# Optimization experiments

Hardware: AMD Instinct MI355X
Metric: run time of the kernel (lower is better)

Reference implementation:

```python
import jax, jax.numpy as jnp
import numpy as np

N_NODES = 50000
N_EDGES = 1600000
D = 64


def setup_inputs() -> dict:
    key = jax.random.key(0)
    ks = jax.random.split(key, 7)
    scale = 1.0 / np.sqrt(2 * D)  # keep activations sane through relu stack
    x = jax.random.normal(ks[0], (N_NODES, D), dtype=jnp.float32)
    edge_index = jax.random.randint(ks[1], (2, N_EDGES), 0, N_NODES, dtype=jnp.int32)
    edge_weight = jax.random.uniform(ks[2], (N_EDGES,), dtype=jnp.float32)
    W1 = jax.random.normal(ks[3], (D, 2 * D), dtype=jnp.float32) * scale
    b1 = jax.random.normal(ks[4], (D,), dtype=jnp.float32) * 0.01
    W2 = jax.random.normal(ks[5], (D, 2 * D), dtype=jnp.float32) * scale
    b2 = jax.random.normal(ks[6], (D,), dtype=jnp.float32) * 0.01
    return {"x": x, "edge_index": edge_index, "edge_weight": edge_weight,
            "W1": W1, "b1": b1, "W2": W2, "b2": b2}


def _sage_conv(x, src, dst, edge_weight, W, b):
    # gather neighbor features, weight, scatter-mean onto src nodes
    m = x[dst] * edge_weight[:, None]                      # [E, d]
    agg_sum = jax.ops.segment_sum(m, src, num_segments=x.shape[0])
    cnt = jax.ops.segment_sum(jnp.ones_like(edge_weight), src,
                              num_segments=x.shape[0])
    agg = agg_sum / jnp.maximum(cnt, 1.0)[:, None]          # scatter 'mean'
    h = jnp.concatenate([x, agg], axis=1)                   # [N, 2d]
    return h @ W.T + b


def reference(x, edge_index, edge_weight, W1, b1, W2, b2):
    src, dst = edge_index[0], edge_index[1]
    h = jax.nn.relu(_sage_conv(x, src, dst, edge_weight, W1, b1))
    h = jax.nn.relu(_sage_conv(h, src, dst, edge_weight, W2, b2))
    return h
```

## Files before the change

kernel.cpp:

```cpp
#include <hip/hip_runtime.h>

#define NN 50000
#define NE 1600000
#define DD 64
#define NPB 196
#define NBKT 256
#define CHUNK 2500
#define NBLK 640
#define SLOT 24
#define SSTR 25
#define S1CAP 1024
#define SPCAP 512
#define CSRCAP 8192

typedef __attribute__((ext_vector_type(8))) short bf16x8;
typedef __attribute__((ext_vector_type(4))) float f32x4;
typedef __attribute__((ext_vector_type(2))) float f32x2;

static __device__ __forceinline__ unsigned short f2bf(float f) {
    unsigned int u = __float_as_uint(f);
    unsigned int r = (u + 0x7FFFu + ((u >> 16) & 1u)) >> 16;
    return (unsigned short)r;
}
static __device__ __forceinline__ float bf2f(unsigned short h) {
    return __uint_as_float((unsigned int)h << 16);
}
static __device__ __forceinline__ unsigned int pk_fp8x4(float a, float b, float c, float d) {
    unsigned int p = __builtin_amdgcn_cvt_pk_fp8_f32(a, b, 0u, false);
    p = __builtin_amdgcn_cvt_pk_fp8_f32(c, d, p, true);
    return p;
}

__global__ __launch_bounds__(256) void prep(
    const float* __restrict__ x, ushort* __restrict__ xb,
    unsigned int* __restrict__ xf8,
    const float* __restrict__ W1, const float* __restrict__ W2,
    ushort* __restrict__ W1b, ushort* __restrict__ W2b,
    int* __restrict__ gcur)
{
    int b = blockIdx.x, tid = threadIdx.x;
    if (b < 3125) {
        int i = b * 256 + tid;
        float4 v = ((const float4*)x)[i];
        ushort4 o;
        o.x = f2bf(v.x); o.y = f2bf(v.y); o.z = f2bf(v.z); o.w = f2bf(v.w);
        ((ushort4*)xb)[i] = o;
        xf8[i] = pk_fp8x4(v.x, v.y, v.z, v.w);
    } else if (b < 3141) {
        int i = (b - 3125) * 256 + tid;
        const float* src = (i < 2048) ? W1 : W2;
        ushort* dst = (i < 2048) ? W1b : W2b;
        int j = i & 2047;
        float4 v = ((const float4*)src)[j];
        ushort4 o;
        o.x = f2bf(v.x); o.y = f2bf(v.y); o.z = f2bf(v.z); o.w = f2bf(v.w);
        ((ushort4*)dst)[j] = o;
    } else {
        for (int i = tid; i < 2304; i += 256) gcur[i] = 0;
    }
}

__global__ __launch_bounds__(256) void bin_lds(
    const int* __restrict__ ei, const float* __restrict__ ew,
    int* __restrict__ gcur, int* __restrict__ gspillc,
    int2* __restrict__ buf1, int2* __restrict__ spill)
{
    __shared__ int2 slot[NBKT * SSTR];
    __shared__ int  lcnt[NBKT];
    __shared__ int  lbase[NBKT];
    int tid = threadIdx.x;
    int shard = blockIdx.x & 7;

    for (int b = tid; b < NBKT; b += 256) lcnt[b] = 0;
    __syncthreads();

    int e0 = blockIdx.x * CHUNK;
    for (int i = tid; i < CHUNK; i += 256) {
        int e = e0 + i;
        int s = ei[e];
        int d = ei[NE + e];
        float w = ew[e];
        int bkt = s / NPB;
        int sloc = s - bkt * NPB;
        int2 rec = make_int2(d | ((int)f2bf(w) << 16), sloc);
        int pos = atomicAdd(&lcnt[bkt], 1);
        if (pos < SLOT) {
            slot[bkt * SSTR + pos] = rec;
        } else {
            int sp = atomicAdd(&gspillc[bkt], 1);
            if (sp < SPCAP) spill[bkt * SPCAP + sp] = rec;
        }
    }
    __syncthreads();

    {
        int b = tid;
        int n = lcnt[b]; if (n > SLOT) n = SLOT;
        lcnt[b] = n;
        lbase[b] = (n > 0) ? atomicAdd(&gcur[b * 8 + shard], n) : 0;
    }
    __syncthreads();

    int wave = tid >> 6, lane = tid & 63;
    int b0 = wave * 64;
    int vcnt = lcnt[b0 + lane];
    int vbase = lbase[b0 + lane];
#pragma unroll 8
    for (int j = 0; j < 64; ++j) {
        int n = __shfl(vcnt, j);
        int base = __shfl(vbase, j);
        int b = b0 + j;
        if (lane < n) {
            int2 rec = slot[b * SSTR + lane];
            int p = base + lane;
            if (p < S1CAP) {
                buf1[((size_t)b * 8 + shard) * S1CAP + p] = rec;
            } else {
                int sp = atomicAdd(&gspillc[b], 1);
                if (sp < SPCAP) spill[b * SPCAP + sp] = rec;
            }
        }
    }
}

__global__ __launch_bounds__(1024) void build_csr(
    const int* __restrict__ gcur, const int2* __restrict__ buf1,
    const int* __restrict__ gspillc, const int2* __restrict__ spill,
    unsigned int* __restrict__ csr, int2* __restrict__ rc)
{
    __shared__ int lcnt[NPB];
    __shared__ int lstart[NPB];
    __shared__ int sa[256], sb[256];
    int tid = threadIdx.x, bkt = blockIdx.x;

    if (tid < NPB) lcnt[tid] = 0;
    __syncthreads();

    for (int sh = 0; sh < 9; ++sh) {
        int n; const int2* rp;
        if (sh < 8) {
            n = gcur[bkt * 8 + sh]; if (n > S1CAP) n = S1CAP;
            rp = buf1 + ((size_t)bkt * 8 + sh) * S1CAP;
        } else {
            n = gspillc[bkt]; if (n > SPCAP) n = SPCAP;
            rp = spill + (size_t)bkt * SPCAP;
        }
        for (int i = tid; i < n; i += 1024)
            atomicAdd(&lcnt[rp[i].y], 1);
    }
    __syncthreads();

    if (tid < 256) sa[tid] = (tid < NPB) ? ((lcnt[tid] + 3) & ~3) : 0;
    __syncthreads();
    int* s = sa; int* d = sb;
    for (int off = 1; off < 256; off <<= 1) {
        if (tid < 256) d[tid] = s[tid] + (tid >= off ? s[tid - off] : 0);
        __syncthreads();
        int* t = s; s = d; d = t;
    }
    if (tid < NPB) {
        int ex = (tid == 0) ? 0 : s[tid - 1];
        lstart[tid] = ex;
        int node = bkt * NPB + tid;
        if (node < NN)
            rc[node] = make_int2(bkt * CSRCAP + ex, lcnt[tid]);
    }
    __syncthreads();
    if (tid < NPB) lcnt[tid] = 0;
    __syncthreads();

    for (int sh = 0; sh < 9; ++sh) {
        int n; const int2* rp;
        if (sh < 8) {
            n = gcur[bkt * 8 + sh]; if (n > S1CAP) n = S1CAP;
            rp = buf1 + ((size_t)bkt * 8 + sh) * S1CAP;
        } else {
            n = gspillc[bkt]; if (n > SPCAP) n = SPCAP;
            rp = spill + (size_t)bkt * SPCAP;
        }
        for (int i = tid; i < n; i += 1024) {
            int2 r = rp[i];
            int pos = atomicAdd(&lcnt[r.y], 1);
            csr[bkt * CSRCAP + lstart[r.y] + pos] = (unsigned int)r.x;
        }
    }
    __syncthreads();

    if (tid < NPB) {
        int c = lcnt[tid];
        int c4 = (c + 3) & ~3;
        for (int p = c; p < c4; ++p)
            csr[bkt * CSRCAP + lstart[tid] + p] = 0u;
    }
}

__global__ __launch_bounds__(256) void aggregate(
    const unsigned int* __restrict__ f8,
    const int2* __restrict__ rc, const unsigned int* __restrict__ csr,
    ushort* __restrict__ aggb)
{
    int node = (blockIdx.x * 256 + threadIdx.x) >> 6;
    int lane = threadIdx.x & 63;
    int g = lane >> 4, l16 = lane & 15;
    int2 rcv = rc[node];
    int n = rcv.y;
    int n4 = (n + 3) & ~3;
    const unsigned int* __restrict__ rp = csr + rcv.x;
    float a0 = 0.f, a1 = 0.f, a2 = 0.f, a3 = 0.f;

    int i = 0;
    for (; i + 16 <= n4; i += 16) {
        uint4 r = *(const uint4*)(rp + i + g * 4);
        unsigned int v0 = f8[(r.x & 0xFFFF) * 16 + l16];
        unsigned int v1 = f8[(r.y & 0xFFFF) * 16 + l16];
        unsigned int v2 = f8[(r.z & 0xFFFF) * 16 + l16];
        unsigned int v3 = f8[(r.w & 0xFFFF) * 16 + l16];
        float w0 = bf2f((unsigned short)(r.x >> 16));
        float w1 = bf2f((unsigned short)(r.y >> 16));
        float w2 = bf2f((unsigned short)(r.z >> 16));
        float w3 = bf2f((unsigned short)(r.w >> 16));
        f32x2 lo, hi;
        lo = __builtin_amdgcn_cvt_pk_f32_fp8(v0, false);
        hi = __builtin_amdgcn_cvt_pk_f32_fp8(v0, true);
        a0 += w0 * lo.x; a1 += w0 * lo.y; a2 += w0 * hi.x; a3 += w0 * hi.y;
        lo = __builtin_amdgcn_cvt_pk_f32_fp8(v1, false);
        hi = __builtin_amdgcn_cvt_pk_f32_fp8(v1, true);
        a0 += w1 * lo.x; a1 += w1 * lo.y; a2 += w1 * hi.x; a3 += w1 * hi.y;
        lo = __builtin_amdgcn_cvt_pk_f32_fp8(v2, false);
        hi = __builtin_amdgcn_cvt_pk_f32_fp8(v2, true);
        a0 += w2 * lo.x; a1 += w2 * lo.y; a2 += w2 * hi.x; a3 += w2 * hi.y;
        lo = __builtin_amdgcn_cvt_pk_f32_fp8(v3, false);
        hi = __builtin_amdgcn_cvt_pk_f32_fp8(v3, true);
        a0 += w3 * lo.x; a1 += w3 * lo.y; a2 += w3 * hi.x; a3 += w3 * hi.y;
    }
    for (; i < n4; i += 4) {
        uint4 r = *(const uint4*)(rp + i);
        unsigned int e = (g == 0) ? r.x : (g == 1) ? r.y : (g == 2) ? r.z : r.w;
        unsigned int v = f8[(e & 0xFFFF) * 16 + l16];
        float w = bf2f((unsigned short)(e >> 16));
        f32x2 lo = __builtin_amdgcn_cvt_pk_f32_fp8(v, false);
        f32x2 hi = __builtin_amdgcn_cvt_pk_f32_fp8(v, true);
        a0 += w * lo.x; a1 += w * lo.y; a2 += w * hi.x; a3 += w * hi.y;
    }

    a0 += __shfl_xor(a0, 16); a0 += __shfl_xor(a0, 32);
    a1 += __shfl_xor(a1, 16); a1 += __shfl_xor(a1, 32);
    a2 += __shfl_xor(a2, 16); a2 += __shfl_xor(a2, 32);
    a3 += __shfl_xor(a3, 16); a3 += __shfl_xor(a3, 32);

    if (lane < 16) {
        float dm = (float)(n > 1 ? n : 1);
        ushort4 o;
        o.x = f2bf(a0 / dm); o.y = f2bf(a1 / dm);
        o.z = f2bf(a2 / dm); o.w = f2bf(a3 / dm);
        *(ushort4*)&aggb[(size_t)node * DD + l16 * 4] = o;
    }
}

__global__ __launch_bounds__(256) void sage_gemm_mfma(
    const ushort* __restrict__ X, const ushort* __restrict__ A,
    const ushort* __restrict__ Wb, const float* __restrict__ bias,
    float* __restrict__ out, ushort* __restrict__ outb,
    unsigned char* __restrict__ outf8)
{
    int tid = threadIdx.x;
    int wave = tid >> 6, lane = tid & 63;
    int quad = lane >> 4, l16 = lane & 15;
    int m0 = blockIdx.x * 64 + wave * 16;

    int arow = m0 + l16; if (arow >= NN) arow = NN - 1;
    const ushort* __restrict__ ax = X + (size_t)arow * DD;
    const ushort* __restrict__ aa = A + (size_t)arow * DD;

    f32x4 acc[4];
#pragma unroll
    for (int t = 0; t < 4; ++t) acc[t] = (f32x4){0.f, 0.f, 0.f, 0.f};

#pragma unroll
    for (int ki = 0; ki < 4; ++ki) {
        const ushort* ap = (ki < 2) ? (ax + ki * 32 + quad * 8)
                                    : (aa + (ki - 2) * 32 + quad * 8);
        bf16x8 af = *(const bf16x8*)ap;
#pragma unroll
        for (int t = 0; t < 4; ++t) {
            const ushort* bp = Wb + (size_t)(t * 16 + l16) * 128 + ki * 32 + quad * 8;
            bf16x8 bfrag = *(const bf16x8*)bp;
            acc[t] = __builtin_amdgcn_mfma_f32_16x16x32_bf16(af, bfrag, acc[t], 0, 0, 0);
        }
    }

#pragma unroll
    for (int t = 0; t < 4; ++t) {
        int col = t * 16 + l16;
        float bv = bias[col];
#pragma unroll
        for (int r = 0; r < 4; ++r) {
            int grow = m0 + quad * 4 + r;
            if (grow < NN) {
                float v = fmaxf(acc[t][r] + bv, 0.f);
                if (out)  out[(size_t)grow * DD + col] = v;
                if (outb) outb[(size_t)grow * DD + col] = f2bf(v);
                if (outf8) {
                    unsigned int p = __builtin_amdgcn_cvt_pk_fp8_f32(v, v, 0u, false);
                    outf8[(size_t)grow * DD + col] = (unsigned char)(p & 0xFFu);
                }
            }
        }
    }
}

extern "C" void kernel_launch(void* const* d_in, const int* in_sizes, int n_in,
                              void* d_out, int out_size, void* d_ws, size_t ws_size,
                              hipStream_t stream)
{
    const float* x  = (const float*)d_in[0];
    const int*   ei = (const int*)d_in[1];
    const float* ew = (const float*)d_in[2];
    const float* W1 = (const float*)d_in[3];
    const float* b1 = (const float*)d_in[4];
    const float* W2 = (const float*)d_in[5];
    const float* b2 = (const float*)d_in[6];
    float* out = (float*)d_out;

    char* ws = (char*)d_ws;
    int*          gcur    = (int*)ws;
    int*          gspillc = (int*)(ws + 8192);
    int2*         buf1    = (int2*)(ws + 16384);
    int2*         spill   = (int2*)(ws + 16793600);
    unsigned int* csr     = (unsigned int*)(ws + 17842176);
    int2*         rc      = (int2*)(ws + 26230784);
    ushort*       xb      = (ushort*)(ws + 26632192);
    ushort*       aggb    = (ushort*)(ws + 33032192);
    ushort*       h1b     = (ushort*)(ws + 39432192);
    ushort*       W1b     = (ushort*)(ws + 45832192);
    ushort*       W2b     = (ushort*)(ws + 45848576);
    unsigned int* xf8     = (unsigned int*)(ws + 45864960);
    unsigned char* h1f8   = (unsigned char*)(ws + 49064960);

    prep<<<3142, 256, 0, stream>>>(x, xb, xf8, W1, W2, W1b, W2b, gcur);
    bin_lds<<<NBLK, 256, 0, stream>>>(ei, ew, gcur, gspillc, buf1, spill);
    build_csr<<<NBKT, 1024, 0, stream>>>(gcur, buf1, gspillc, spill, csr, rc);

    aggregate<<<(NN * 64) / 256, 256, 0, stream>>>(xf8, rc, csr, aggb);
    sage_gemm_mfma<<<(NN + 63) / 64, 256, 0, stream>>>(xb, aggb, W1b, b1, nullptr, h1b, h1f8);

    aggregate<<<(NN * 64) / 256, 256, 0, stream>>>((const unsigned int*)h1f8, rc, csr, aggb);
    sage_gemm_mfma<<<(NN + 63) / 64, 256, 0, stream>>>(h1b, aggb, W2b, b2, out, nullptr, nullptr);
}
```

Baseline: 202.2 us.

## Fuse neighbor aggregation with MFMA linear layer per 16-node block

Merges the aggregate and GEMM kernels into one 1024-thread kernel. Each of its 16 waves aggregates one node into LDS, then 4 waves run the 16x64 MFMA tile from LDS. This removes the aggb global round trip and two kernel launches per layer. In exchange, 12 of 16 waves sit idle during the GEMM phase, blocks sync on their slowest node's degree, and every block reloads the weight fragments.

After: 199.2 us. No clear change (-1.5%).

```diff
diff --git a/kernel.cpp b/kernel.cpp
--- a/kernel.cpp
+++ b/kernel.cpp
@@ -194,14 +194,26 @@
     }
 }
 
-__global__ __launch_bounds__(256) void aggregate(
+__global__ __launch_bounds__(1024) void fused_layer(
+    const ushort* __restrict__ Xb,
     const unsigned int* __restrict__ f8,
     const int2* __restrict__ rc, const unsigned int* __restrict__ csr,
-    ushort* __restrict__ aggb)
-{
-    int node = (blockIdx.x * 256 + threadIdx.x) >> 6;
-    int lane = threadIdx.x & 63;
+    const ushort* __restrict__ Wb, const float* __restrict__ bias,
+    float* __restrict__ out, ushort* __restrict__ outb,
+    unsigned char* __restrict__ outf8)
+{
+    __shared__ ushort xL[16][72];
+    __shared__ ushort aggL[16][72];
+    int tid = threadIdx.x;
+    int wave = tid >> 6, lane = tid & 63;
     int g = lane >> 4, l16 = lane & 15;
+    int base = blockIdx.x * 16;
+    int node = base + wave;
+
+    if (lane < 16)
+        *(ushort4*)&xL[wave][l16 * 4] =
+            *(const ushort4*)&Xb[(size_t)node * DD + l16 * 4];
+
     int2 rcv = rc[node];
     int n = rcv.y;
     int n4 = (n + 3) & ~3;
@@ -253,57 +265,31 @@
         ushort4 o;
         o.x = f2bf(a0 / dm); o.y = f2bf(a1 / dm);
         o.z = f2bf(a2 / dm); o.w = f2bf(a3 / dm);
-        *(ushort4*)&aggb[(size_t)node * DD + l16 * 4] = o;
-    }
-}
-
-__global__ __launch_bounds__(256) void sage_gemm_mfma(
-    const ushort* __restrict__ X, const ushort* __restrict__ A,
-    const ushort* __restrict__ Wb, const float* __restrict__ bias,
-    float* __restrict__ out, ushort* __restrict__ outb,
-    unsigned char* __restrict__ outf8)
-{
-    int tid = threadIdx.x;
-    int wave = tid >> 6, lane = tid & 63;
-    int quad = lane >> 4, l16 = lane & 15;
-    int m0 = blockIdx.x * 64 + wave * 16;
-
-    int arow = m0 + l16; if (arow >= NN) arow = NN - 1;
-    const ushort* __restrict__ ax = X + (size_t)arow * DD;
-    const ushort* __restrict__ aa = A + (size_t)arow * DD;
-
-    f32x4 acc[4];
+        *(ushort4*)&aggL[wave][l16 * 4] = o;
+    }
+    __syncthreads();
+
+    if (wave < 4) {
+        f32x4 acc = (f32x4){0.f, 0.f, 0.f, 0.f};
 #pragma unroll
-    for (int t = 0; t < 4; ++t) acc[t] = (f32x4){0.f, 0.f, 0.f, 0.f};
-
-#pragma unroll
-    for (int ki = 0; ki < 4; ++ki) {
-        const ushort* ap = (ki < 2) ? (ax + ki * 32 + quad * 8)
-                                    : (aa + (ki - 2) * 32 + quad * 8);
-        bf16x8 af = *(const bf16x8*)ap;
-#pragma unroll
-        for (int t = 0; t < 4; ++t) {
-            const ushort* bp = Wb + (size_t)(t * 16 + l16) * 128 + ki * 32 + quad * 8;
-            bf16x8 bfrag = *(const bf16x8*)bp;
-            acc[t] = __builtin_amdgcn_mfma_f32_16x16x32_bf16(af, bfrag, acc[t], 0, 0, 0);
-        }
-    }
-
-#pragma unroll
-    for (int t = 0; t < 4; ++t) {
-        int col = t * 16 + l16;
+        for (int ki = 0; ki < 4; ++ki) {
+            const ushort* ap = (ki < 2) ? &xL[l16][ki * 32 + g * 8]
+                                        : &aggL[l16][(ki - 2) * 32 + g * 8];
+            bf16x8 af = *(const bf16x8*)ap;
+            bf16x8 bfrag = *(const bf16x8*)&Wb[(size_t)(wave * 16 + l16) * 128 + ki * 32 + g * 8];
+            acc = __builtin_amdgcn_mfma_f32_16x16x32_bf16(af, bfrag, acc, 0, 0, 0);
+        }
+        int col = wave * 16 + l16;
         float bv = bias[col];
 #pragma unroll
         for (int r = 0; r < 4; ++r) {
-            int grow = m0 + quad * 4 + r;
-            if (grow < NN) {
-                float v = fmaxf(acc[t][r] + bv, 0.f);
-                if (out)  out[(size_t)grow * DD + col] = v;
-                if (outb) outb[(size_t)grow * DD + col] = f2bf(v);
-                if (outf8) {
-                    unsigned int p = __builtin_amdgcn_cvt_pk_fp8_f32(v, v, 0u, false);
-                    outf8[(size_t)grow * DD + col] = (unsigned char)(p & 0xFFu);
-                }
+            int grow = base + g * 4 + r;
+            float v = fmaxf(acc[r] + bv, 0.f);
+            if (out)  out[(size_t)grow * DD + col] = v;
+            if (outb) outb[(size_t)grow * DD + col] = f2bf(v);
+            if (outf8) {
+                unsigned int p = __builtin_amdgcn_cvt_pk_fp8_f32(v, v, 0u, false);
+                outf8[(size_t)grow * DD + col] = (unsigned char)(p & 0xFFu);
             }
         }
     }
@@ -330,7 +316,6 @@
     unsigned int* csr     = (unsigned int*)(ws + 17842176);
     int2*         rc      = (int2*)(ws + 26230784);
     ushort*       xb      = (ushort*)(ws + 26632192);
-    ushort*       aggb    = (ushort*)(ws + 33032192);
     ushort*       h1b     = (ushort*)(ws + 39432192);
     ushort*       W1b     = (ushort*)(ws + 45832192);
     ushort*       W2b     = (ushort*)(ws + 45848576);
@@ -341,9 +326,8 @@
     bin_lds<<<NBLK, 256, 0, stream>>>(ei, ew, gcur, gspillc, buf1, spill);
     build_csr<<<NBKT, 1024, 0, stream>>>(gcur, buf1, gspillc, spill, csr, rc);
 
-    aggregate<<<(NN * 64) / 256, 256, 0, stream>>>(xf8, rc, csr, aggb);
-    sage_gemm_mfma<<<(NN + 63) / 64, 256, 0, stream>>>(xb, aggb, W1b, b1, nullptr, h1b, h1f8);
-
-    aggregate<<<(NN * 64) / 256, 256, 0, stream>>>((const unsigned int*)h1f8, rc, csr, aggb);
-    sage_gemm_mfma<<<(NN + 63) / 64, 256, 0, stream>>>(h1b, aggb, W2b, b2, out, nullptr, nullptr);
-}
+    fused_layer<<<NN / 16, 1024, 0, stream>>>(xb, xf8, rc, csr, W1b, b1,
+                                              nullptr, h1b, h1f8);
+    fused_layer<<<NN / 16, 1024, 0, stream>>>(h1b, (const unsigned int*)h1f8,
+                                              rc, csr, W2b, b2, out, nullptr, nullptr);
+}
```
